# Performance work log

Measured on AMD Instinct MI355X. Metric: run time of the kernel, lower is better.

The kernel has to match this reference:

```python
import jax, jax.numpy as jnp
import numpy as np

PAD = 10000.0  # sentinel value marking invalid fg points


def setup_inputs() -> dict:
    key = jax.random.key(0)
    k1, k2, k3 = jax.random.split(key, 3)
    B, N, M, D = 8, 4096, 4096, 3
    fg = jax.random.normal(k1, (B, N, D), dtype=jnp.float32)
    prj = jax.random.normal(k2, (B, M, D), dtype=jnp.float32)
    # per-sample valid lengths in [1, N]; pad the tail rows with the sentinel
    x_lengths = jax.random.randint(k3, (B,), 1, N + 1)
    row_idx = jnp.arange(N)[None, :]              # [1, N]
    pad_mask = row_idx >= x_lengths[:, None]      # [B, N] True where padded
    fg = jnp.where(pad_mask[:, :, None], PAD, fg)
    return {"fg_points": fg, "prj_points": prj, "x_lengths": x_lengths}


def _chamfer(fg, prj):
    # fg: [B, N, 3] (padded with PAD rows), prj: [B, M, 3]
    valid = jnp.all(fg != PAD, axis=-1)  # [B, N]
    # squared pairwise distances via ||a||^2 + ||b||^2 - 2 a.b  -> [B, N, M]
    d2 = (jnp.sum(fg * fg, axis=-1)[:, :, None]
          + jnp.sum(prj * prj, axis=-1)[:, None, :]
          - 2.0 * jnp.einsum('bnd,bmd->bnm', fg, prj))
    d2 = jnp.maximum(d2, 0.0)
    n_valid = jnp.sum(valid, axis=1).astype(jnp.float32)  # [B]
    # x -> y: min over prj for each valid fg point, mean over valid points
    cham_x = jnp.sum(jnp.where(valid, jnp.min(d2, axis=2), 0.0), axis=1) / n_valid
    # y -> x: min over valid fg points for each prj point, mean over prj
    BIG = jnp.float32(1e30)
    cham_y = jnp.mean(jnp.min(jnp.where(valid[:, :, None], d2, BIG), axis=1), axis=1)
    # pytorch3d chamfer_distance (default reductions) = cham_x + cham_y per sample
    return jnp.mean(cham_x + cham_y)


def reference(fg_points, prj_points, x_lengths):
    fg = fg_points.astype(jnp.float32)
    prj = prj_points.astype(jnp.float32)
    _ = x_lengths.astype(jnp.int64)  # cast, unused (matches original)
    return _chamfer(fg, prj)
```

## Files before the change

kernel.cpp:

```cpp
#include <hip/hip_runtime.h>

#define TPB 256
#define PPT 8
#define OWN_TILE (TPB * PPT)
#define CHUNK 128

__global__ void cham_init_kernel(unsigned int* __restrict__ mins, int count,
                                 float* __restrict__ out) {
    int i = blockIdx.x * blockDim.x + threadIdx.x;
    if (i < count) mins[i] = 0x7F800000u;
    if (i == 0) out[0] = 0.f;
}

__global__ __launch_bounds__(TPB) void cham_dist_kernel(
    const float* __restrict__ fg, const float* __restrict__ prj,
    unsigned int* __restrict__ rowmin, unsigned int* __restrict__ colmin,
    int B, int N, int M,
    int tilesX, int chunksX, int tilesY, int chunksY)
{
    const int blocksX = B * tilesX * chunksX;
    int idx = blockIdx.x;
    const int side = (idx >= blocksX) ? 1 : 0;
    if (side) idx -= blocksX;
    const int tilesPer  = side ? tilesY  : tilesX;
    const int chunksPer = side ? chunksY : chunksX;
    const int b     = idx / (tilesPer * chunksPer);
    const int rem   = idx % (tilesPer * chunksPer);
    const int tile  = rem / chunksPer;
    const int chunk = rem % chunksPer;

    const float* own     = side ? prj : fg;
    const float* other   = side ? fg  : prj;
    unsigned int* outArr = side ? colmin : rowmin;
    const int ownCount   = side ? M : N;
    const int otherCount = side ? N : M;

    const int base = tile * OWN_TILE;
    float m2x[PPT], m2y[PPT], m2z[PPT], aa[PPT], mn[PPT];
    #pragma unroll
    for (int p = 0; p < PPT; ++p) {
        int i = base + p * TPB + threadIdx.x;
        int li = (i < ownCount) ? i : (ownCount - 1);
        const float* a = own + ((size_t)b * ownCount + li) * 3;
        float ax = a[0], ay = a[1], az = a[2];
        m2x[p] = -2.f * ax; m2y[p] = -2.f * ay; m2z[p] = -2.f * az;
        aa[p]  = ax * ax + ay * ay + az * az;
        mn[p]  = __int_as_float(0x7F800000);
    }

    const int start = chunk * CHUNK;
    const int cnt   = min(CHUNK, otherCount - start);
    __shared__ float4 tilebuf[CHUNK];
    if (threadIdx.x < cnt) {
        const float* q = other + ((size_t)b * otherCount + start + threadIdx.x) * 3;
        float bx = q[0], by = q[1], bz = q[2];
        tilebuf[threadIdx.x] = make_float4(bx, by, bz, bx * bx + by * by + bz * bz);
    }
    __syncthreads();

    #pragma unroll 4
    for (int j = 0; j < cnt; ++j) {
        float4 q = tilebuf[j];
        #pragma unroll
        for (int p = 0; p < PPT; ++p) {
            float t = fmaf(m2x[p], q.x, q.w);
            t = fmaf(m2y[p], q.y, t);
            t = fmaf(m2z[p], q.z, t);
            mn[p] = fminf(mn[p], t);
        }
    }

    #pragma unroll
    for (int p = 0; p < PPT; ++p) {
        int i = base + p * TPB + threadIdx.x;
        if (i < ownCount) {
            float v = fmaxf(mn[p] + aa[p], 0.f);
            atomicMin(&outArr[(size_t)b * ownCount + i], __float_as_uint(v));
        }
    }
}

__global__ __launch_bounds__(256) void cham_reduce_kernel(
    const unsigned int* __restrict__ rowmin, const unsigned int* __restrict__ colmin,
    const int* __restrict__ lengths, float* __restrict__ out, int B, int N, int M)
{
    __shared__ float wavesum[4];
    const int b    = blockIdx.x;
    const int tid  = threadIdx.x;
    const int lane = tid & 63;
    const int wave = tid >> 6;

    const int L = lengths[b];
    float sx = 0.f, sy = 0.f;
    for (int n = tid; n < L; n += 256) sx += __uint_as_float(rowmin[(size_t)b * N + n]);
    for (int m = tid; m < M; m += 256) sy += __uint_as_float(colmin[(size_t)b * M + m]);
    float v = sx / (float)L + sy / (float)M;
    #pragma unroll
    for (int off = 32; off > 0; off >>= 1) v += __shfl_down(v, off, 64);
    if (lane == 0) wavesum[wave] = v;
    __syncthreads();
    if (tid == 0) {
        float total = wavesum[0] + wavesum[1] + wavesum[2] + wavesum[3];
        atomicAdd(out, total / (float)B);
    }
}

extern "C" void kernel_launch(void* const* d_in, const int* in_sizes, int n_in,
                              void* d_out, int out_size, void* d_ws, size_t ws_size,
                              hipStream_t stream) {
    const float* fg      = (const float*)d_in[0];
    const float* prj     = (const float*)d_in[1];
    const int*   lengths = (const int*)d_in[2];
    float*       out     = (float*)d_out;

    const int B = in_sizes[2];
    const int N = in_sizes[0] / (3 * B);
    const int M = in_sizes[1] / (3 * B);

    unsigned int* rowmin = (unsigned int*)d_ws;
    unsigned int* colmin = rowmin + (size_t)B * N;

    const int totalMins = B * (N + M);
    cham_init_kernel<<<(totalMins + 255) / 256, 256, 0, stream>>>(rowmin, totalMins, out);

    const int tilesX  = (N + OWN_TILE - 1) / OWN_TILE;
    const int chunksX = (M + CHUNK - 1) / CHUNK;
    const int tilesY  = (M + OWN_TILE - 1) / OWN_TILE;
    const int chunksY = (N + CHUNK - 1) / CHUNK;
    const int totalBlocks = B * (tilesX * chunksX + tilesY * chunksY);
    cham_dist_kernel<<<totalBlocks, TPB, 0, stream>>>(
        fg, prj, rowmin, colmin, B, N, M, tilesX, chunksX, tilesY, chunksY);

    cham_reduce_kernel<<<B, 256, 0, stream>>>(rowmin, colmin, lengths, out, B, N, M);
}
```

Before: 86.93 us.

## Skip distance work for padded fg points using x_lengths per sample

Passes the per-sample valid lengths into the distance kernel so that padded fg points are never processed. Whole chunks past the valid length are dropped on the prj side, and whole waves past it are dropped on the fg side. Each wave now owns a contiguous span of points, and the inner loop is unrolled over two other-points at a time to shorten the min dependency chain. This relies on x_lengths matching the PAD sentinel layout, where the reference instead detects padding by value.

```diff
diff --git a/kernel.cpp b/kernel.cpp
--- a/kernel.cpp
+++ b/kernel.cpp
@@ -2,6 +2,7 @@
 
 #define TPB 256
 #define PPT 8
+#define WAVE_OWN (64 * PPT)
 #define OWN_TILE (TPB * PPT)
 #define CHUNK 128
 
@@ -14,6 +15,7 @@
 
 __global__ __launch_bounds__(TPB) void cham_dist_kernel(
     const float* __restrict__ fg, const float* __restrict__ prj,
+    const int* __restrict__ lengths,
     unsigned int* __restrict__ rowmin, unsigned int* __restrict__ colmin,
     int B, int N, int M,
     int tilesX, int chunksX, int tilesY, int chunksY)
@@ -34,22 +36,15 @@
     unsigned int* outArr = side ? colmin : rowmin;
     const int ownCount   = side ? M : N;
     const int otherCount = side ? N : M;
+    const int L          = lengths[b];
 
-    const int base = tile * OWN_TILE;
-    float m2x[PPT], m2y[PPT], m2z[PPT], aa[PPT], mn[PPT];
-    #pragma unroll
-    for (int p = 0; p < PPT; ++p) {
-        int i = base + p * TPB + threadIdx.x;
-        int li = (i < ownCount) ? i : (ownCount - 1);
-        const float* a = own + ((size_t)b * ownCount + li) * 3;
-        float ax = a[0], ay = a[1], az = a[2];
-        m2x[p] = -2.f * ax; m2y[p] = -2.f * ay; m2z[p] = -2.f * az;
-        aa[p]  = ax * ax + ay * ay + az * az;
-        mn[p]  = __int_as_float(0x7F800000);
+    const int start = chunk * CHUNK;
+    int cnt = min(CHUNK, otherCount - start);
+    if (side == 1) {
+        if (start >= L) return;
+        cnt = min(cnt, L - start);
     }
 
-    const int start = chunk * CHUNK;
-    const int cnt   = min(CHUNK, otherCount - start);
     __shared__ float4 tilebuf[CHUNK];
     if (threadIdx.x < cnt) {
         const float* q = other + ((size_t)b * otherCount + start + threadIdx.x) * 3;
@@ -58,21 +53,54 @@
     }
     __syncthreads();
 
-    #pragma unroll 4
-    for (int j = 0; j < cnt; ++j) {
-        float4 q = tilebuf[j];
+    const int lane  = threadIdx.x & 63;
+    const int wave  = threadIdx.x >> 6;
+    const int wbase = tile * OWN_TILE + wave * WAVE_OWN;
+    if (wbase >= ownCount) return;
+    if (side == 0 && wbase >= L) return;
+
+    float m2x[PPT], m2y[PPT], m2z[PPT], aa[PPT], mn[PPT];
+    #pragma unroll
+    for (int p = 0; p < PPT; ++p) {
+        int i  = wbase + p * 64 + lane;
+        int li = min(i, ownCount - 1);
+        const float* a = own + ((size_t)b * ownCount + li) * 3;
+        float ax = a[0], ay = a[1], az = a[2];
+        m2x[p] = -2.f * ax; m2y[p] = -2.f * ay; m2z[p] = -2.f * az;
+        aa[p]  = ax * ax + ay * ay + az * az;
+        mn[p]  = __int_as_float(0x7F800000);
+    }
+
+    int j = 0;
+    #pragma unroll 2
+    for (; j + 1 < cnt; j += 2) {
+        float4 q0 = tilebuf[j];
+        float4 q1 = tilebuf[j + 1];
         #pragma unroll
         for (int p = 0; p < PPT; ++p) {
-            float t = fmaf(m2x[p], q.x, q.w);
-            t = fmaf(m2y[p], q.y, t);
-            t = fmaf(m2z[p], q.z, t);
-            mn[p] = fminf(mn[p], t);
+            float t0 = fmaf(m2x[p], q0.x, q0.w);
+            t0 = fmaf(m2y[p], q0.y, t0);
+            t0 = fmaf(m2z[p], q0.z, t0);
+            float t1 = fmaf(m2x[p], q1.x, q1.w);
+            t1 = fmaf(m2y[p], q1.y, t1);
+            t1 = fmaf(m2z[p], q1.z, t1);
+            mn[p] = fminf(fminf(t0, t1), mn[p]);
+        }
+    }
+    if (j < cnt) {
+        float4 q0 = tilebuf[j];
+        #pragma unroll
+        for (int p = 0; p < PPT; ++p) {
+            float t0 = fmaf(m2x[p], q0.x, q0.w);
+            t0 = fmaf(m2y[p], q0.y, t0);
+            t0 = fmaf(m2z[p], q0.z, t0);
+            mn[p] = fminf(mn[p], t0);
         }
     }
 
     #pragma unroll
     for (int p = 0; p < PPT; ++p) {
-        int i = base + p * TPB + threadIdx.x;
+        int i = wbase + p * 64 + lane;
         if (i < ownCount) {
             float v = fmaxf(mn[p] + aa[p], 0.f);
             atomicMin(&outArr[(size_t)b * ownCount + i], __float_as_uint(v));
@@ -129,7 +157,7 @@
     const int chunksY = (N + CHUNK - 1) / CHUNK;
     const int totalBlocks = B * (tilesX * chunksX + tilesY * chunksY);
     cham_dist_kernel<<<totalBlocks, TPB, 0, stream>>>(
-        fg, prj, rowmin, colmin, B, N, M, tilesX, chunksX, tilesY, chunksY);
+        fg, prj, lengths, rowmin, colmin, B, N, M, tilesX, chunksX, tilesY, chunksY);
 
     cham_reduce_kernel<<<B, 256, 0, stream>>>(rowmin, colmin, lengths, out, B, N, M);
 }
```

New measurement: 84.21 us. -3.1%, faster.
